# Optimization experiments

Hardware: AMD Instinct MI355X
Metric: run time of the kernel (lower is better)

Reference implementation:

```python
import jax, jax.numpy as jnp
import numpy as np


def setup_inputs() -> dict:
    key = jax.random.key(0)
    ks = jax.random.split(key, 6)
    B, S, I, H, O = 64, 2048, 256, 256, 256
    x = jax.random.normal(ks[0], (B, S, I), dtype=jnp.float32)
    # nn.Linear stores weight as [out_features, in_features]; y = x @ W.T
    W_ih = jax.random.normal(ks[1], (H, I), dtype=jnp.float32) / np.sqrt(I)
    W_hh = jax.random.normal(ks[2], (H, H), dtype=jnp.float32) / np.sqrt(H)
    b_h = jnp.zeros((H,), dtype=jnp.float32)
    W_ho = jax.random.normal(ks[3], (O, H), dtype=jnp.float32) / np.sqrt(H)
    b_o = jax.random.normal(ks[4], (O,), dtype=jnp.float32) / np.sqrt(H)
    return {"x": x, "W_ih": W_ih, "W_hh": W_hh, "b_h": b_h, "W_ho": W_ho, "b_o": b_o}


def reference(x, W_ih, W_hh, b_h, W_ho, b_o):
    B, S, I = x.shape
    H = W_hh.shape[0]
    # Precompute input projection for all timesteps in one GEMM: [B,S,H]
    xW = jnp.einsum('bsi,hi->bsh', x, W_ih) + b_h

    def step(h, xw_t):
        h = jnp.tanh(xw_t + h @ W_hh.T)  # [B,H]
        out = h @ W_ho.T + b_o           # [B,O]
        return h, out

    h0 = jnp.zeros((B, H), dtype=x.dtype)
    # scan over time axis: move S to leading dim
    h_final, outs = jax.lax.scan(step, h0, jnp.swapaxes(xW, 0, 1))
    outputs = jnp.swapaxes(outs, 0, 1)  # [B,S,O]
    return (outputs, h_final)
```

## Files before the change

kernel.cpp:

```cpp
#include <hip/hip_runtime.h>
#include <hip/hip_bf16.h>

#define Bdim 64
#define Sdim 2048
#define Hdim 256

typedef __attribute__((ext_vector_type(8))) short short8;
typedef __attribute__((ext_vector_type(4))) float f32x4;

static __device__ __forceinline__ unsigned short f2bf(float f) {
  union { float f; unsigned int u; } v; v.f = f;
  unsigned int r = v.u + 0x7fffu + ((v.u >> 16) & 1u);
  return (unsigned short)(r >> 16);
}
static __device__ __forceinline__ float bf2f(unsigned short u) {
  union { unsigned int u; float f; } v; v.u = ((unsigned int)u) << 16;
  return v.f;
}
static __device__ __forceinline__ float bflo(unsigned int u) {
  union { unsigned int u; float f; } v; v.u = u << 16; return v.f;
}
static __device__ __forceinline__ float bfhi(unsigned int u) {
  union { unsigned int u; float f; } v; v.u = u & 0xffff0000u; return v.f;
}

#if __has_builtin(__builtin_amdgcn_rcpf)
#define FAST_RCP(x) __builtin_amdgcn_rcpf(x)
#else
#define FAST_RCP(x) (1.0f / (x))
#endif

static __device__ __forceinline__ float tanh_fast(float x) {
  float ax = fabsf(x);
  float e = exp2f(ax * -2.8853900817779268f);
  float r = (1.0f - e) * FAST_RCP(1.0f + e);
  return copysignf(r, x);
}

template<int XW_F32>
__global__ __launch_bounds__(512, 1) void rnn_scan_mfma(
    const void* __restrict__ xwp, const float* __restrict__ Whh,
    float* __restrict__ hout, float* __restrict__ hfin) {
  __shared__ __align__(16) unsigned short hbuf[2][16 * 256];
  const int tid = threadIdx.x;
  const int lane = tid & 63;
  const int wv = tid >> 6;
  const int l15 = lane & 15;
  const int g = lane >> 4;
  const int bs = blockIdx.x * 16;

  for (int i = tid; i < 16 * 256; i += 512) hbuf[0][i] = 0;

  short8 bfrag[2][8];
#pragma unroll
  for (int tau = 0; tau < 2; ++tau) {
    int n = wv * 32 + tau * 16 + l15;
#pragma unroll
    for (int ks = 0; ks < 8; ++ks) {
      int k0 = ks * 32 + g * 8;
      const float* p = Whh + n * 256 + k0;
      short8 v;
#pragma unroll
      for (int e = 0; e < 8; ++e) v[e] = (short)f2bf(p[e]);
      bfrag[tau][ks] = v;
    }
  }

  int aroff[8];
#pragma unroll
  for (int ks = 0; ks < 8; ++ks)
    aroff[ks] = l15 * 512 + ((ks * 64 + g * 16) ^ ((l15 & 7) << 4));

  long base[2][4];
  int woff[2][4];
  int fidx[2][4];
#pragma unroll
  for (int tau = 0; tau < 2; ++tau) {
#pragma unroll
    for (int e = 0; e < 4; ++e) {
      int m = g * 4 + e;
      int n = wv * 32 + tau * 16 + l15;
      base[tau][e] = ((long)(bs + m) * Sdim) * Hdim + n;
      woff[tau][e] = m * 512 + ((n * 2) ^ ((m & 7) << 4));
      fidx[tau][e] = (bs + m) * Hdim + n;
    }
  }

  const float* xwf = (const float*)xwp;
  const unsigned short* xwh = (const unsigned short*)xwp;

  float xwA[2][4], xwB[2][4];
#pragma unroll
  for (int tau = 0; tau < 2; ++tau)
#pragma unroll
    for (int e = 0; e < 4; ++e) {
      xwA[tau][e] = XW_F32 ? xwf[base[tau][e]] : bf2f(xwh[base[tau][e]]);
      xwB[tau][e] = XW_F32 ? xwf[base[tau][e] + Hdim] : bf2f(xwh[base[tau][e] + Hdim]);
    }

  __syncthreads();

  int cb = 0;
  auto step = [&](int tc, float (&buf)[2][4]) {
    f32x4 acc0, acc1;
#pragma unroll
    for (int e = 0; e < 4; ++e) { acc0[e] = buf[0][e]; acc1[e] = buf[1][e]; }

    const int tn = (tc + 2 < Sdim) ? tc + 2 : Sdim - 1;
#pragma unroll
    for (int tau = 0; tau < 2; ++tau)
#pragma unroll
      for (int e = 0; e < 4; ++e)
        buf[tau][e] = XW_F32 ? xwf[base[tau][e] + (long)tn * Hdim]
                             : bf2f(xwh[base[tau][e] + (long)tn * Hdim]);

    const char* hb = (const char*)hbuf[cb];
#pragma unroll
    for (int ks = 0; ks < 8; ++ks) {
      short8 a = *(const short8*)(hb + aroff[ks]);
      acc0 = __builtin_amdgcn_mfma_f32_16x16x32_bf16(a, bfrag[0][ks], acc0, 0, 0, 0);
      acc1 = __builtin_amdgcn_mfma_f32_16x16x32_bf16(a, bfrag[1][ks], acc1, 0, 0, 0);
    }

    char* hn = (char*)hbuf[cb ^ 1];
#pragma unroll
    for (int tau = 0; tau < 2; ++tau) {
#pragma unroll
      for (int e = 0; e < 4; ++e) {
        float v = tanh_fast(tau == 0 ? acc0[e] : acc1[e]);
        *(unsigned short*)(hn + woff[tau][e]) = f2bf(v);
        hout[base[tau][e] + (long)tc * Hdim] = v;
        if (tc == Sdim - 1) hfin[fidx[tau][e]] = v;
      }
    }

    __builtin_amdgcn_sched_barrier(0);
    asm volatile("s_waitcnt lgkmcnt(0)" ::: "memory");
    __builtin_amdgcn_s_barrier();
    __builtin_amdgcn_sched_barrier(0);
    cb ^= 1;
  };

  for (int t = 0; t < Sdim; t += 2) {
    step(t, xwA);
    step(t + 1, xwB);
  }
}

__global__ __launch_bounds__(256, 1) void rnn_scan_valu_fused(
    const float* __restrict__ x, const float* __restrict__ Wih,
    const float* __restrict__ bh, const float* __restrict__ Whh,
    float* __restrict__ hout, float* __restrict__ hfin) {
  __shared__ __align__(16) uint2 wt[64][256];
  __shared__ __align__(16) float hl[256];
  const int n = threadIdx.x;
  const int b = blockIdx.x;
  {
    const float2* src = (const float2*)Whh;
    unsigned int* w32 = (unsigned int*)wt;
    for (int i = n; i < 32768; i += 256) {
      float2 f = src[i];
      unsigned int u = (unsigned int)f2bf(f.x) | ((unsigned int)f2bf(f.y) << 16);
      int row = i >> 7, kk = i & 127, k4 = kk >> 1, half = kk & 1;
      w32[k4 * 512 + row * 2 + half] = u;
    }
  }
  hl[n] = 0.0f;
  __syncthreads();
  const long base = (long)b * Sdim * Hdim + n;
  for (int t = 0; t < Sdim; ++t) {
    const float* xr = x + ((long)b * Sdim + t) * 256;
    const float* wr = Wih + n * 256;
    float acc = bh[n];
    for (int k = 0; k < 256; ++k) acc += xr[k] * wr[k];
#pragma unroll 8
    for (int k4 = 0; k4 < 64; ++k4) {
      uint2 w2 = wt[k4][n];
      float4 h4 = *(const float4*)&hl[k4 * 4];
      acc += bflo(w2.x) * h4.x + bfhi(w2.x) * h4.y
           + bflo(w2.y) * h4.z + bfhi(w2.y) * h4.w;
    }
    float hv = tanh_fast(acc);
    __syncthreads();
    hl[n] = hv;
    hout[base + (long)t * Hdim] = hv;
    if (t == Sdim - 1) hfin[b * Hdim + n] = hv;
    __syncthreads();
  }
}

template<int A_F32, int OUT_F32>
__global__ __launch_bounds__(512, 2) void gemm256(const void* __restrict__ Ap,
                                                  const float* __restrict__ Wf,
                                                  const float* __restrict__ bias,
                                                  void* __restrict__ outp) {
  __shared__ __align__(16) char wl[131072];
  const int tid = threadIdx.x;
  const int lane = tid & 63;
  const int wv = tid >> 6;
  const int l15 = lane & 15;
  const int g = lane >> 4;
  const long r0 = (long)blockIdx.x * 128;

  for (int i = tid; i < 256 * 64; i += 512) {
    int n = i >> 6;
    int kc = (i & 63) * 4;
    f32x4 c = *(const f32x4*)(Wf + n * 256 + kc);
    unsigned int lo = (unsigned int)f2bf(c[0]) | ((unsigned int)f2bf(c[1]) << 16);
    unsigned int hi = (unsigned int)f2bf(c[2]) | ((unsigned int)f2bf(c[3]) << 16);
    int kb = (kc * 2) ^ ((n & 7) << 4);
    unsigned int* dst = (unsigned int*)(wl + n * 512 + kb);
    dst[0] = lo; dst[1] = hi;
  }
  __syncthreads();

  f32x4 acc[16];
#pragma unroll
  for (int tau = 0; tau < 16; ++tau) {
    float bv = bias[tau * 16 + l15];
    acc[tau][0] = bv; acc[tau][1] = bv; acc[tau][2] = bv; acc[tau][3] = bv;
  }

  const long arow = r0 + wv * 16 + l15;
#pragma unroll
  for (int ks = 0; ks < 8; ++ks) {
    const int k0 = ks * 32 + g * 8;
    short8 a;
    if (A_F32) {
      const f32x4* ap = (const f32x4*)((const float*)Ap + arow * 256 + k0);
      f32x4 x0 = ap[0], x1 = ap[1];
#pragma unroll
      for (int e = 0; e < 4; ++e) { a[e] = (short)f2bf(x0[e]); a[4 + e] = (short)f2bf(x1[e]); }
    } else {
      a = *(const short8*)((const unsigned short*)Ap + arow * 256 + k0);
    }
#pragma unroll
    for (int tau = 0; tau < 16; ++tau) {
      int n = tau * 16 + l15;
      int kb = (k0 * 2) ^ ((n & 7) << 4);
      short8 b = *(const short8*)(wl + n * 512 + kb);
      acc[tau] = __builtin_amdgcn_mfma_f32_16x16x32_bf16(a, b, acc[tau], 0, 0, 0);
    }
  }

#pragma unroll
  for (int tau = 0; tau < 16; ++tau) {
    int n = tau * 16 + l15;
#pragma unroll
    for (int e = 0; e < 4; ++e) {
      long row = r0 + wv * 16 + g * 4 + e;
      if (OUT_F32) ((float*)outp)[row * 256 + n] = acc[tau][e];
      else         ((unsigned short*)outp)[row * 256 + n] = f2bf(acc[tau][e]);
    }
  }
}

extern "C" void kernel_launch(void* const* d_in, const int* in_sizes, int n_in,
                              void* d_out, int out_size, void* d_ws, size_t ws_size,
                              hipStream_t stream) {
  const float* x    = (const float*)d_in[0];
  const float* W_ih = (const float*)d_in[1];
  const float* W_hh = (const float*)d_in[2];
  const float* b_h  = (const float*)d_in[3];
  const float* W_ho = (const float*)d_in[4];
  const float* b_o  = (const float*)d_in[5];
  float* out  = (float*)d_out;
  float* hout = out;
  float* hfin = out + (size_t)Bdim * Sdim * Hdim;

  const int gblocks = (Bdim * Sdim) / 128;
  const size_t need32 = (size_t)Bdim * Sdim * Hdim * 4;
  const size_t need16 = need32 / 2;

  if (ws_size >= need32) {
    gemm256<1, 1><<<gblocks, 512, 0, stream>>>(x, W_ih, b_h, d_ws);
    rnn_scan_mfma<1><<<4, 512, 0, stream>>>(d_ws, W_hh, hout, hfin);
  } else if (ws_size >= need16) {
    gemm256<1, 0><<<gblocks, 512, 0, stream>>>(x, W_ih, b_h, d_ws);
    rnn_scan_mfma<0><<<4, 512, 0, stream>>>(d_ws, W_hh, hout, hfin);
  } else {
    rnn_scan_valu_fused<<<Bdim, 256, 0, stream>>>(x, W_ih, b_h, W_hh, hout, hfin);
  }
  gemm256<1, 1><<<gblocks, 512, 0, stream>>>(hout, W_ho, b_o, out);
}
```

Measured before the change: 2.135 ms.

## Transpose MFMA operands so each lane owns contiguous hidden units, vectorizing I/O

```diff
diff --git a/kernel.cpp b/kernel.cpp
--- a/kernel.cpp
+++ b/kernel.cpp
@@ -31,10 +31,8 @@
 #endif
 
 static __device__ __forceinline__ float tanh_fast(float x) {
-  float ax = fabsf(x);
-  float e = exp2f(ax * -2.8853900817779268f);
-  float r = (1.0f - e) * FAST_RCP(1.0f + e);
-  return copysignf(r, x);
+  float e = exp2f(x * 2.8853900817779268f);
+  return 1.0f - 2.0f * FAST_RCP(1.0f + e);
 }
 
 template<int XW_F32>
@@ -51,7 +49,7 @@
 
   for (int i = tid; i < 16 * 256; i += 512) hbuf[0][i] = 0;
 
-  short8 bfrag[2][8];
+  short8 wfrag[2][8];
 #pragma unroll
   for (int tau = 0; tau < 2; ++tau) {
     int n = wv * 32 + tau * 16 + l15;
@@ -62,7 +60,7 @@
       short8 v;
 #pragma unroll
       for (int e = 0; e < 8; ++e) v[e] = (short)f2bf(p[e]);
-      bfrag[tau][ks] = v;
+      wfrag[tau][ks] = v;
     }
   }
 
@@ -71,67 +69,80 @@
   for (int ks = 0; ks < 8; ++ks)
     aroff[ks] = l15 * 512 + ((ks * 64 + g * 16) ^ ((l15 & 7) << 4));
 
-  long base[2][4];
-  int woff[2][4];
-  int fidx[2][4];
-#pragma unroll
-  for (int tau = 0; tau < 2; ++tau) {
-#pragma unroll
-    for (int e = 0; e < 4; ++e) {
-      int m = g * 4 + e;
-      int n = wv * 32 + tau * 16 + l15;
-      base[tau][e] = ((long)(bs + m) * Sdim) * Hdim + n;
-      woff[tau][e] = m * 512 + ((n * 2) ^ ((m & 7) << 4));
-      fidx[tau][e] = (bs + m) * Hdim + n;
-    }
-  }
+  const int nb0 = wv * 32 + g * 4;
+  const int nb1 = nb0 + 16;
+  const long rowbase = (long)(bs + l15) * Sdim * Hdim;
 
   const float* xwf = (const float*)xwp;
   const unsigned short* xwh = (const unsigned short*)xwp;
 
-  float xwA[2][4], xwB[2][4];
-#pragma unroll
-  for (int tau = 0; tau < 2; ++tau)
-#pragma unroll
-    for (int e = 0; e < 4; ++e) {
-      xwA[tau][e] = XW_F32 ? xwf[base[tau][e]] : bf2f(xwh[base[tau][e]]);
-      xwB[tau][e] = XW_F32 ? xwf[base[tau][e] + Hdim] : bf2f(xwh[base[tau][e] + Hdim]);
-    }
+  const int wo0 = l15 * 512 + ((2 * nb0) ^ ((l15 & 7) << 4));
+  const int wo1 = l15 * 512 + ((2 * nb1) ^ ((l15 & 7) << 4));
+
+  f32x4 xwA0, xwA1, xwB0, xwB1;
+  {
+    long i0 = rowbase + nb0, i1 = rowbase + nb1;
+    if (XW_F32) {
+      xwA0 = *(const f32x4*)(xwf + i0);          xwA1 = *(const f32x4*)(xwf + i1);
+      xwB0 = *(const f32x4*)(xwf + i0 + Hdim);   xwB1 = *(const f32x4*)(xwf + i1 + Hdim);
+    } else {
+      ushort4 a0 = *(const ushort4*)(xwh + i0), a1 = *(const ushort4*)(xwh + i1);
+      ushort4 b0 = *(const ushort4*)(xwh + i0 + Hdim), b1 = *(const ushort4*)(xwh + i1 + Hdim);
+      xwA0[0]=bf2f(a0.x); xwA0[1]=bf2f(a0.y); xwA0[2]=bf2f(a0.z); xwA0[3]=bf2f(a0.w);
+      xwA1[0]=bf2f(a1.x); xwA1[1]=bf2f(a1.y); xwA1[2]=bf2f(a1.z); xwA1[3]=bf2f(a1.w);
+      xwB0[0]=bf2f(b0.x); xwB0[1]=bf2f(b0.y); xwB0[2]=bf2f(b0.z); xwB0[3]=bf2f(b0.w);
+      xwB1[0]=bf2f(b1.x); xwB1[1]=bf2f(b1.y); xwB1[2]=bf2f(b1.z); xwB1[3]=bf2f(b1.w);
+    }
+  }
 
   __syncthreads();
 
   int cb = 0;
-  auto step = [&](int tc, float (&buf)[2][4]) {
-    f32x4 acc0, acc1;
-#pragma unroll
-    for (int e = 0; e < 4; ++e) { acc0[e] = buf[0][e]; acc1[e] = buf[1][e]; }
-
-    const int tn = (tc + 2 < Sdim) ? tc + 2 : Sdim - 1;
-#pragma unroll
-    for (int tau = 0; tau < 2; ++tau)
-#pragma unroll
-      for (int e = 0; e < 4; ++e)
-        buf[tau][e] = XW_F32 ? xwf[base[tau][e] + (long)tn * Hdim]
-                             : bf2f(xwh[base[tau][e] + (long)tn * Hdim]);
+  auto step = [&](int tc, f32x4& buf0, f32x4& buf1) {
+    f32x4 acc0 = buf0, acc1 = buf1;
+
+    const long tn = (tc + 2 < Sdim) ? tc + 2 : Sdim - 1;
+    {
+      long i0 = rowbase + tn * Hdim + nb0, i1 = rowbase + tn * Hdim + nb1;
+      if (XW_F32) {
+        buf0 = *(const f32x4*)(xwf + i0);
+        buf1 = *(const f32x4*)(xwf + i1);
+      } else {
+        ushort4 a0 = *(const ushort4*)(xwh + i0), a1 = *(const ushort4*)(xwh + i1);
+        buf0[0]=bf2f(a0.x); buf0[1]=bf2f(a0.y); buf0[2]=bf2f(a0.z); buf0[3]=bf2f(a0.w);
+        buf1[0]=bf2f(a1.x); buf1[1]=bf2f(a1.y); buf1[2]=bf2f(a1.z); buf1[3]=bf2f(a1.w);
+      }
+    }
 
     const char* hb = (const char*)hbuf[cb];
 #pragma unroll
     for (int ks = 0; ks < 8; ++ks) {
-      short8 a = *(const short8*)(hb + aroff[ks]);
-      acc0 = __builtin_amdgcn_mfma_f32_16x16x32_bf16(a, bfrag[0][ks], acc0, 0, 0, 0);
-      acc1 = __builtin_amdgcn_mfma_f32_16x16x32_bf16(a, bfrag[1][ks], acc1, 0, 0, 0);
+      short8 b = *(const short8*)(hb + aroff[ks]);
+      acc0 = __builtin_amdgcn_mfma_f32_16x16x32_bf16(wfrag[0][ks], b, acc0, 0, 0, 0);
+      acc1 = __builtin_amdgcn_mfma_f32_16x16x32_bf16(wfrag[1][ks], b, acc1, 0, 0, 0);
     }
 
     char* hn = (char*)hbuf[cb ^ 1];
-#pragma unroll
-    for (int tau = 0; tau < 2; ++tau) {
-#pragma unroll
-      for (int e = 0; e < 4; ++e) {
-        float v = tanh_fast(tau == 0 ? acc0[e] : acc1[e]);
-        *(unsigned short*)(hn + woff[tau][e]) = f2bf(v);
-        hout[base[tau][e] + (long)tc * Hdim] = v;
-        if (tc == Sdim - 1) hfin[fidx[tau][e]] = v;
-      }
+    f32x4 v0, v1;
+#pragma unroll
+    for (int e = 0; e < 4; ++e) v0[e] = tanh_fast(acc0[e]);
+#pragma unroll
+    for (int e = 0; e < 4; ++e) v1[e] = tanh_fast(acc1[e]);
+
+    unsigned int p00, p01, p10, p11;
+    asm("v_cvt_pk_bf16_f32 %0, %1, %2" : "=v"(p00) : "v"(v0[0]), "v"(v0[1]));
+    asm("v_cvt_pk_bf16_f32 %0, %1, %2" : "=v"(p01) : "v"(v0[2]), "v"(v0[3]));
+    asm("v_cvt_pk_bf16_f32 %0, %1, %2" : "=v"(p10) : "v"(v1[0]), "v"(v1[1]));
+    asm("v_cvt_pk_bf16_f32 %0, %1, %2" : "=v"(p11) : "v"(v1[2]), "v"(v1[3]));
+    *(uint2*)(hn + wo0) = make_uint2(p00, p01);
+    *(uint2*)(hn + wo1) = make_uint2(p10, p11);
+
+    const long ob = rowbase + (long)tc * Hdim;
+    *(f32x4*)(hout + ob + nb0) = v0;
+    *(f32x4*)(hout + ob + nb1) = v1;
+    if (tc == Sdim - 1) {
+      *(f32x4*)(hfin + (bs + l15) * Hdim + nb0) = v0;
+      *(f32x4*)(hfin + (bs + l15) * Hdim + nb1) = v1;
     }
 
     __builtin_amdgcn_sched_barrier(0);
@@ -142,8 +153,8 @@
   };
 
   for (int t = 0; t < Sdim; t += 2) {
-    step(t, xwA);
-    step(t + 1, xwB);
+    step(t, xwA0, xwA1);
+    step(t + 1, xwB0, xwB1);
   }
 }
 
```

New measurement: 2.538 ms. 18.9% more time.

## Transpose MFMA operands in RNN scan, halve waves, vectorize xW/h I/O

Applied to the files above, without the earlier changes.

```diff
diff --git a/kernel.cpp b/kernel.cpp
--- a/kernel.cpp
+++ b/kernel.cpp
@@ -31,14 +31,12 @@
 #endif
 
 static __device__ __forceinline__ float tanh_fast(float x) {
-  float ax = fabsf(x);
-  float e = exp2f(ax * -2.8853900817779268f);
-  float r = (1.0f - e) * FAST_RCP(1.0f + e);
-  return copysignf(r, x);
+  float e = exp2f(x * 2.8853900817779268f);
+  return 1.0f - 2.0f * FAST_RCP(1.0f + e);
 }
 
 template<int XW_F32>
-__global__ __launch_bounds__(512, 1) void rnn_scan_mfma(
+__global__ __launch_bounds__(256, 1) void rnn_scan_mfma(
     const void* __restrict__ xwp, const float* __restrict__ Whh,
     float* __restrict__ hout, float* __restrict__ hfin) {
   __shared__ __align__(16) unsigned short hbuf[2][16 * 256];
@@ -49,12 +47,12 @@
   const int g = lane >> 4;
   const int bs = blockIdx.x * 16;
 
-  for (int i = tid; i < 16 * 256; i += 512) hbuf[0][i] = 0;
-
-  short8 bfrag[2][8];
-#pragma unroll
-  for (int tau = 0; tau < 2; ++tau) {
-    int n = wv * 32 + tau * 16 + l15;
+  for (int i = tid; i < 16 * 256; i += 256) hbuf[0][i] = 0;
+
+  short8 wfrag[4][8];
+#pragma unroll
+  for (int tau = 0; tau < 4; ++tau) {
+    int n = wv * 64 + tau * 16 + l15;
 #pragma unroll
     for (int ks = 0; ks < 8; ++ks) {
       int k0 = ks * 32 + g * 8;
@@ -62,7 +60,7 @@
       short8 v;
 #pragma unroll
       for (int e = 0; e < 8; ++e) v[e] = (short)f2bf(p[e]);
-      bfrag[tau][ks] = v;
+      wfrag[tau][ks] = v;
     }
   }
 
@@ -71,67 +69,66 @@
   for (int ks = 0; ks < 8; ++ks)
     aroff[ks] = l15 * 512 + ((ks * 64 + g * 16) ^ ((l15 & 7) << 4));
 
-  long base[2][4];
-  int woff[2][4];
-  int fidx[2][4];
-#pragma unroll
-  for (int tau = 0; tau < 2; ++tau) {
-#pragma unroll
-    for (int e = 0; e < 4; ++e) {
-      int m = g * 4 + e;
-      int n = wv * 32 + tau * 16 + l15;
-      base[tau][e] = ((long)(bs + m) * Sdim) * Hdim + n;
-      woff[tau][e] = m * 512 + ((n * 2) ^ ((m & 7) << 4));
-      fidx[tau][e] = (bs + m) * Hdim + n;
-    }
-  }
+  int nb[4], wo[4];
+#pragma unroll
+  for (int tau = 0; tau < 4; ++tau) {
+    nb[tau] = wv * 64 + tau * 16 + g * 4;
+    wo[tau] = l15 * 512 + ((2 * nb[tau]) ^ ((l15 & 7) << 4));
+  }
+  const long rowbase = (long)(bs + l15) * Sdim * Hdim;
 
   const float* xwf = (const float*)xwp;
   const unsigned short* xwh = (const unsigned short*)xwp;
 
-  float xwA[2][4], xwB[2][4];
-#pragma unroll
-  for (int tau = 0; tau < 2; ++tau)
-#pragma unroll
-    for (int e = 0; e < 4; ++e) {
-      xwA[tau][e] = XW_F32 ? xwf[base[tau][e]] : bf2f(xwh[base[tau][e]]);
-      xwB[tau][e] = XW_F32 ? xwf[base[tau][e] + Hdim] : bf2f(xwh[base[tau][e] + Hdim]);
-    }
+  auto ldxw = [&](long idx) -> f32x4 {
+    if (XW_F32) return *(const f32x4*)(xwf + idx);
+    ushort4 a = *(const ushort4*)(xwh + idx);
+    f32x4 r; r[0]=bf2f(a.x); r[1]=bf2f(a.y); r[2]=bf2f(a.z); r[3]=bf2f(a.w);
+    return r;
+  };
+
+  f32x4 bufA[4], bufB[4];
+#pragma unroll
+  for (int tau = 0; tau < 4; ++tau) {
+    bufA[tau] = ldxw(rowbase + nb[tau]);
+    bufB[tau] = ldxw(rowbase + Hdim + nb[tau]);
+  }
 
   __syncthreads();
 
   int cb = 0;
-  auto step = [&](int tc, float (&buf)[2][4]) {
-    f32x4 acc0, acc1;
-#pragma unroll
-    for (int e = 0; e < 4; ++e) { acc0[e] = buf[0][e]; acc1[e] = buf[1][e]; }
-
-    const int tn = (tc + 2 < Sdim) ? tc + 2 : Sdim - 1;
-#pragma unroll
-    for (int tau = 0; tau < 2; ++tau)
-#pragma unroll
-      for (int e = 0; e < 4; ++e)
-        buf[tau][e] = XW_F32 ? xwf[base[tau][e] + (long)tn * Hdim]
-                             : bf2f(xwh[base[tau][e] + (long)tn * Hdim]);
+  auto step = [&](int tc, f32x4 (&buf)[4]) {
+    f32x4 acc[4];
+#pragma unroll
+    for (int tau = 0; tau < 4; ++tau) acc[tau] = buf[tau];
+
+    const long tn = (tc + 2 < Sdim) ? tc + 2 : Sdim - 1;
+#pragma unroll
+    for (int tau = 0; tau < 4; ++tau)
+      buf[tau] = ldxw(rowbase + tn * Hdim + nb[tau]);
 
     const char* hb = (const char*)hbuf[cb];
 #pragma unroll
     for (int ks = 0; ks < 8; ++ks) {
-      short8 a = *(const short8*)(hb + aroff[ks]);
-      acc0 = __builtin_amdgcn_mfma_f32_16x16x32_bf16(a, bfrag[0][ks], acc0, 0, 0, 0);
-      acc1 = __builtin_amdgcn_mfma_f32_16x16x32_bf16(a, bfrag[1][ks], acc1, 0, 0, 0);
+      short8 h8 = *(const short8*)(hb + aroff[ks]);
+#pragma unroll
+      for (int tau = 0; tau < 4; ++tau)
+        acc[tau] = __builtin_amdgcn_mfma_f32_16x16x32_bf16(wfrag[tau][ks], h8, acc[tau], 0, 0, 0);
     }
 
     char* hn = (char*)hbuf[cb ^ 1];
-#pragma unroll
-    for (int tau = 0; tau < 2; ++tau) {
-#pragma unroll
-      for (int e = 0; e < 4; ++e) {
-        float v = tanh_fast(tau == 0 ? acc0[e] : acc1[e]);
-        *(unsigned short*)(hn + woff[tau][e]) = f2bf(v);
-        hout[base[tau][e] + (long)tc * Hdim] = v;
-        if (tc == Sdim - 1) hfin[fidx[tau][e]] = v;
-      }
+    const long ob = rowbase + (long)tc * Hdim;
+#pragma unroll
+    for (int tau = 0; tau < 4; ++tau) {
+      f32x4 v;
+#pragma unroll
+      for (int e = 0; e < 4; ++e) v[e] = tanh_fast(acc[tau][e]);
+      unsigned int plo, phi;
+      asm("v_cvt_pk_bf16_f32 %0, %1, %2" : "=v"(plo) : "v"(v[0]), "v"(v[1]));
+      asm("v_cvt_pk_bf16_f32 %0, %1, %2" : "=v"(phi) : "v"(v[2]), "v"(v[3]));
+      *(uint2*)(hn + wo[tau]) = make_uint2(plo, phi);
+      *(f32x4*)(hout + ob + nb[tau]) = v;
+      if (tc == Sdim - 1) *(f32x4*)(hfin + (bs + l15) * Hdim + nb[tau]) = v;
     }
 
     __builtin_amdgcn_sched_barrier(0);
@@ -142,8 +139,8 @@
   };
 
   for (int t = 0; t < Sdim; t += 2) {
-    step(t, xwA);
-    step(t + 1, xwB);
+    step(t, bufA);
+    step(t + 1, bufB);
   }
 }
 
@@ -274,10 +271,10 @@
 
   if (ws_size >= need32) {
     gemm256<1, 1><<<gblocks, 512, 0, stream>>>(x, W_ih, b_h, d_ws);
-    rnn_scan_mfma<1><<<4, 512, 0, stream>>>(d_ws, W_hh, hout, hfin);
+    rnn_scan_mfma<1><<<4, 256, 0, stream>>>(d_ws, W_hh, hout, hfin);
   } else if (ws_size >= need16) {
     gemm256<1, 0><<<gblocks, 512, 0, stream>>>(x, W_ih, b_h, d_ws);
-    rnn_scan_mfma<0><<<4, 512, 0, stream>>>(d_ws, W_hh, hout, hfin);
+    rnn_scan_mfma<0><<<4, 256, 0, stream>>>(d_ws, W_hh, hout, hfin);
   } else {
     rnn_scan_valu_fused<<<Bdim, 256, 0, stream>>>(x, W_ih, b_h, W_hh, hout, hfin);
   }
```

New measurement: 2.399 ms. +12.4%, slower.
